# Performance work log

Hardware: AMD Instinct MI355X
Metric: run time of the kernel (lower is better)

Reference implementation:

```python
import jax, jax.numpy as jnp
import numpy as np

NUM_USERS = 100000
NUM_ITEMS = 50000
IN_DIM = 128
HID_DIM = 256
OUT_DIM = 64
R = 5
E = 300000  # edges per rating level
EPS = 1e-10


def setup_inputs() -> dict:
    key = jax.random.key(0)
    ks = jax.random.split(key, 12)
    # edge lists per rating, regularized to dense [R, E]
    u_idx = jax.random.randint(ks[0], (R, E), 0, NUM_USERS, dtype=jnp.int32)
    v_idx = jax.random.randint(ks[1], (R, E), 0, NUM_ITEMS, dtype=jnp.int32)
    deg_user = jax.random.uniform(ks[2], (NUM_USERS,), dtype=jnp.float32) * 50.0
    deg_item = jax.random.uniform(ks[3], (NUM_ITEMS,), dtype=jnp.float32) * 100.0
    # learned parameters (xavier-ish scaling)
    X_u = jax.random.normal(ks[4], (NUM_USERS, IN_DIM), dtype=jnp.float32) * 0.02
    X_v = jax.random.normal(ks[5], (NUM_ITEMS, IN_DIM), dtype=jnp.float32) * 0.02
    s1 = float(np.sqrt(6.0 / (IN_DIM + HID_DIM)))
    W_item2user = jax.random.uniform(ks[6], (R, IN_DIM, HID_DIM), dtype=jnp.float32, minval=-s1, maxval=s1)
    W_user2item = jax.random.uniform(ks[7], (R, IN_DIM, HID_DIM), dtype=jnp.float32, minval=-s1, maxval=s1)
    s2 = float(np.sqrt(6.0 / (HID_DIM + OUT_DIM)))
    W_out_user = jax.random.uniform(ks[8], (HID_DIM, OUT_DIM), dtype=jnp.float32, minval=-s2, maxval=s2)
    b_out_user = jnp.zeros((OUT_DIM,), dtype=jnp.float32)
    W_out_item = jax.random.uniform(ks[9], (HID_DIM, OUT_DIM), dtype=jnp.float32, minval=-s2, maxval=s2)
    b_out_item = jnp.zeros((OUT_DIM,), dtype=jnp.float32)
    return {
        "u_idx": u_idx, "v_idx": v_idx,
        "deg_user": deg_user, "deg_item": deg_item,
        "X_u": X_u, "X_v": X_v,
        "W_item2user": W_item2user, "W_user2item": W_user2item,
        "W_out_user": W_out_user, "b_out_user": b_out_user,
        "W_out_item": W_out_item, "b_out_item": b_out_item,
    }


def reference(u_idx, v_idx, deg_user, deg_item, X_u, X_v,
              W_item2user, W_user2item,
              W_out_user, b_out_user, W_out_item, b_out_item):
    num_users = X_u.shape[0]
    num_items = X_v.shape[0]
    deg_u = jnp.sqrt(jnp.clip(deg_user, EPS))
    deg_v = jnp.sqrt(jnp.clip(deg_item, EPS))
    # per-edge symmetric normalization, [R, E]
    norm = 1.0 / (deg_u[u_idx] * deg_v[v_idx])
    # gather + per-rating matmul + normalize  ([R,E,in] x [R,in,hid] -> [R,E,hid])
    msgs_to_u = jnp.einsum('rek,rkh->reh', X_v[v_idx], W_item2user) * norm[..., None]
    msgs_to_v = jnp.einsum('rek,rkh->reh', X_u[u_idx], W_user2item) * norm[..., None]
    # scatter-add into shared accumulators (equivalent of index_add_ over all ratings)
    m_u = jax.ops.segment_sum(msgs_to_u.reshape(-1, msgs_to_u.shape[-1]),
                              u_idx.reshape(-1), num_segments=num_users)
    m_v = jax.ops.segment_sum(msgs_to_v.reshape(-1, msgs_to_v.shape[-1]),
                              v_idx.reshape(-1), num_segments=num_items)
    # output dense layers + ReLU (dropout disabled / eval mode)
    h_u = jax.nn.relu(m_u @ W_out_user + b_out_user)
    h_v = jax.nn.relu(m_v @ W_out_item + b_out_item)
    return h_u, h_v
```

## Files before the change

kernel.cpp:

```cpp
#include <hip/hip_runtime.h>
#include <hip/hip_bf16.h>

#define NUM_USERS 100000
#define NUM_ITEMS 50000
#define IN_DIM 128
#define HID_DIM 256
#define OUT_DIM 64
#define R_LEVELS 5
#define NEDGE 300000
#define EPSC 1e-10f

typedef float f32x4 __attribute__((ext_vector_type(4)));
typedef short s16x8 __attribute__((ext_vector_type(8)));

static __device__ __forceinline__ short f2bf(float f) {
    __hip_bfloat16 h = __float2bfloat16(f);
    return *reinterpret_cast<short*>(&h);
}

__global__ void fuse_weights(const float* __restrict__ W_i2u,
                             const float* __restrict__ W_u2i,
                             const float* __restrict__ Wout_u,
                             const float* __restrict__ Wout_i,
                             unsigned short* __restrict__ WcT_u,
                             unsigned short* __restrict__ WcT_v) {
    const int rk = blockIdx.x;
    const int r  = rk >> 7;
    const int k  = rk & 127;
    const int j  = threadIdx.x;
    const bool userDir = (blockIdx.y == 0);
    const float* w1   = (userDir ? W_i2u : W_u2i) + (size_t)rk * HID_DIM;
    const float* wout = (userDir ? Wout_u : Wout_i);
    float acc = 0.f;
    for (int h = 0; h < HID_DIM; ++h)
        acc = fmaf(w1[h], wout[h * OUT_DIM + j], acc);
    unsigned short* dst = (userDir ? WcT_u : WcT_v);
    dst[(((size_t)r * OUT_DIM + j) * IN_DIM) + k] = (unsigned short)f2bf(acc);
}

__global__ __launch_bounds__(256)
void edge_mfma(const int*   __restrict__ u_idx,
               const int*   __restrict__ v_idx,
               const float* __restrict__ deg_user,
               const float* __restrict__ deg_item,
               const float* __restrict__ X_u,
               const float* __restrict__ X_v,
               const unsigned short* __restrict__ WcT_u,
               const unsigned short* __restrict__ WcT_v,
               float*       __restrict__ out) {
    const int r    = blockIdx.y;
    const bool toUser = (blockIdx.z == 0);
    const int lane = threadIdx.x & 63;
    const int wave = threadIdx.x >> 6;
    const int m    = lane & 15;
    const int g    = lane >> 4;

    const int*   dI   = (toUser ? u_idx : v_idx) + (size_t)r * NEDGE;
    const int*   sI   = (toUser ? v_idx : u_idx) + (size_t)r * NEDGE;
    const float* degD = toUser ? deg_user : deg_item;
    const float* degS = toUser ? deg_item : deg_user;
    const float* Xs   = toUser ? X_v : X_u;
    const unsigned short* WcT = (toUser ? WcT_u : WcT_v) + (size_t)r * OUT_DIM * IN_DIM;
    float*       outp = out + (toUser ? 0 : (size_t)NUM_USERS * OUT_DIM);

    s16x8 bfrag[4][4];
#pragma unroll
    for (int nt = 0; nt < 4; ++nt)
#pragma unroll
        for (int ks = 0; ks < 4; ++ks)
            bfrag[nt][ks] = *reinterpret_cast<const s16x8*>(
                WcT + ((size_t)(nt * 16 + m) * IN_DIM + ks * 32 + g * 8));

    const int wid     = blockIdx.x * 4 + wave;
    const int wstride = gridDim.x * 4;
    constexpr int NCHUNK = NEDGE / 16;

    for (int c = wid; c < NCHUNK; c += wstride) {
        const int e0 = c * 16;
        const int   sS  = sI[e0 + m];
        const int   dDm = dI[e0 + m];
        const float norm = 1.0f / (sqrtf(fmaxf(degD[dDm], EPSC)) *
                                   sqrtf(fmaxf(degS[sS],  EPSC)));
        const float* xrow = Xs + (size_t)sS * IN_DIM;

        s16x8 afrag[4];
#pragma unroll
        for (int ks = 0; ks < 4; ++ks) {
            const float4 q0 = *reinterpret_cast<const float4*>(xrow + ks * 32 + g * 8);
            const float4 q1 = *reinterpret_cast<const float4*>(xrow + ks * 32 + g * 8 + 4);
            s16x8 av;
            av[0] = f2bf(q0.x * norm); av[1] = f2bf(q0.y * norm);
            av[2] = f2bf(q0.z * norm); av[3] = f2bf(q0.w * norm);
            av[4] = f2bf(q1.x * norm); av[5] = f2bf(q1.y * norm);
            av[6] = f2bf(q1.z * norm); av[7] = f2bf(q1.w * norm);
            afrag[ks] = av;
        }

        int dd[4];
#pragma unroll
        for (int i = 0; i < 4; ++i) dd[i] = dI[e0 + g * 4 + i];

#pragma unroll
        for (int nt = 0; nt < 4; ++nt) {
            f32x4 acc = {0.f, 0.f, 0.f, 0.f};
#pragma unroll
            for (int ks = 0; ks < 4; ++ks)
                acc = __builtin_amdgcn_mfma_f32_16x16x32_bf16(
                    afrag[ks], bfrag[nt][ks], acc, 0, 0, 0);
#pragma unroll
            for (int i = 0; i < 4; ++i)
                atomicAdd(outp + (size_t)dd[i] * OUT_DIM + nt * 16 + m, acc[i]);
        }
    }
}

__global__ void bias_relu(float* __restrict__ out,
                          const float* __restrict__ b_u,
                          const float* __restrict__ b_v) {
    const size_t i = (size_t)blockIdx.x * 256 + threadIdx.x;
    constexpr size_t UOUT = (size_t)NUM_USERS * OUT_DIM;
    constexpr size_t TOT  = UOUT + (size_t)NUM_ITEMS * OUT_DIM;
    if (i < TOT) {
        const float b = (i < UOUT) ? b_u[i & 63] : b_v[i & 63];
        out[i] = fmaxf(out[i] + b, 0.f);
    }
}

extern "C" void kernel_launch(void* const* d_in, const int* in_sizes, int n_in,
                              void* d_out, int out_size, void* d_ws, size_t ws_size,
                              hipStream_t stream) {
    const int*   u_idx    = (const int*)  d_in[0];
    const int*   v_idx    = (const int*)  d_in[1];
    const float* deg_user = (const float*)d_in[2];
    const float* deg_item = (const float*)d_in[3];
    const float* X_u      = (const float*)d_in[4];
    const float* X_v      = (const float*)d_in[5];
    const float* W_i2u    = (const float*)d_in[6];
    const float* W_u2i    = (const float*)d_in[7];
    const float* W_out_u  = (const float*)d_in[8];
    const float* b_out_u  = (const float*)d_in[9];
    const float* W_out_i  = (const float*)d_in[10];
    const float* b_out_i  = (const float*)d_in[11];

    float* out  = (float*)d_out;
    unsigned short* WcT_u = (unsigned short*)d_ws;
    unsigned short* WcT_v = WcT_u + (size_t)R_LEVELS * OUT_DIM * IN_DIM;

    hipMemsetAsync(d_out, 0, (size_t)out_size * sizeof(float), stream);

    fuse_weights<<<dim3(R_LEVELS * IN_DIM, 2), 64, 0, stream>>>(
        W_i2u, W_u2i, W_out_u, W_out_i, WcT_u, WcT_v);

    edge_mfma<<<dim3(128, R_LEVELS, 2), 256, 0, stream>>>(
        u_idx, v_idx, deg_user, deg_item, X_u, X_v, WcT_u, WcT_v, out);

    const size_t total = (size_t)NUM_USERS * OUT_DIM + (size_t)NUM_ITEMS * OUT_DIM;
    bias_relu<<<(int)((total + 255) / 256), 256, 0, stream>>>(out, b_out_u, b_out_i);
}
```

Measured before the change: 808.3 us.

## Prescale feature rows to bf16 and factor destination degree norm into epilogue

Adds a prescale pass that multiplies each source row by its inverse sqrt degree and stores it as bf16. The destination-side normalization moves out of the edge loop and into the final bias/ReLU pass as a per-row scale. The edge kernel then gathers half-size bf16 rows, skips the per-edge degree lookups and conversions, and loads destination indices as int4. The grid also grows from 128 to 384 blocks in x. This costs an extra pass over both feature tables plus workspace, and the fast path is only taken when the workspace is large enough.

```diff
diff --git a/kernel.cpp b/kernel.cpp
--- a/kernel.cpp
+++ b/kernel.cpp
@@ -13,9 +13,9 @@
 typedef float f32x4 __attribute__((ext_vector_type(4)));
 typedef short s16x8 __attribute__((ext_vector_type(8)));
 
-static __device__ __forceinline__ short f2bf(float f) {
+static __device__ __forceinline__ unsigned short f2bf(float f) {
     __hip_bfloat16 h = __float2bfloat16(f);
-    return *reinterpret_cast<short*>(&h);
+    return *reinterpret_cast<unsigned short*>(&h);
 }
 
 __global__ void fuse_weights(const float* __restrict__ W_i2u,
@@ -35,19 +35,32 @@
     for (int h = 0; h < HID_DIM; ++h)
         acc = fmaf(w1[h], wout[h * OUT_DIM + j], acc);
     unsigned short* dst = (userDir ? WcT_u : WcT_v);
-    dst[(((size_t)r * OUT_DIM + j) * IN_DIM) + k] = (unsigned short)f2bf(acc);
+    dst[(((size_t)r * OUT_DIM + j) * IN_DIM) + k] = f2bf(acc);
+}
+
+__global__ void prescale_rows(const float* __restrict__ X,
+                              const float* __restrict__ deg,
+                              unsigned short* __restrict__ Xn,
+                              float* __restrict__ rsq, int nrows) {
+    const int row = blockIdx.x * 4 + (threadIdx.x >> 6);
+    if (row >= nrows) return;
+    const int lane = threadIdx.x & 63;
+    const float r = 1.0f / sqrtf(fmaxf(deg[row], EPSC));
+    if (lane == 0) rsq[row] = r;
+    const float2 x = ((const float2*)(X + (size_t)row * IN_DIM))[lane];
+    const unsigned int packed = (unsigned int)f2bf(x.x * r) |
+                                ((unsigned int)f2bf(x.y * r) << 16);
+    ((unsigned int*)(Xn + (size_t)row * IN_DIM))[lane] = packed;
 }
 
 __global__ __launch_bounds__(256)
-void edge_mfma(const int*   __restrict__ u_idx,
-               const int*   __restrict__ v_idx,
-               const float* __restrict__ deg_user,
-               const float* __restrict__ deg_item,
-               const float* __restrict__ X_u,
-               const float* __restrict__ X_v,
-               const unsigned short* __restrict__ WcT_u,
-               const unsigned short* __restrict__ WcT_v,
-               float*       __restrict__ out) {
+void edge_mfma_pre(const int* __restrict__ u_idx,
+                   const int* __restrict__ v_idx,
+                   const unsigned short* __restrict__ Xn_u,
+                   const unsigned short* __restrict__ Xn_v,
+                   const unsigned short* __restrict__ WcT_u,
+                   const unsigned short* __restrict__ WcT_v,
+                   float* __restrict__ out) {
     const int r    = blockIdx.y;
     const bool toUser = (blockIdx.z == 0);
     const int lane = threadIdx.x & 63;
@@ -55,13 +68,71 @@
     const int m    = lane & 15;
     const int g    = lane >> 4;
 
+    const int* dI = (toUser ? u_idx : v_idx) + (size_t)r * NEDGE;
+    const int* sI = (toUser ? v_idx : u_idx) + (size_t)r * NEDGE;
+    const unsigned short* Xn  = toUser ? Xn_v : Xn_u;
+    const unsigned short* WcT = (toUser ? WcT_u : WcT_v) + (size_t)r * OUT_DIM * IN_DIM;
+    float* outp = out + (toUser ? 0 : (size_t)NUM_USERS * OUT_DIM);
+
+    s16x8 bfrag[4][4];
+#pragma unroll
+    for (int nt = 0; nt < 4; ++nt)
+#pragma unroll
+        for (int ks = 0; ks < 4; ++ks)
+            bfrag[nt][ks] = *reinterpret_cast<const s16x8*>(
+                WcT + ((size_t)(nt * 16 + m) * IN_DIM + ks * 32 + g * 8));
+
+    const int wid     = blockIdx.x * 4 + wave;
+    const int wstride = gridDim.x * 4;
+    constexpr int NCHUNK = NEDGE / 16;
+
+    for (int c = wid; c < NCHUNK; c += wstride) {
+        const int e0 = c * 16;
+        const int sS = sI[e0 + m];
+        const int4 dd4 = *reinterpret_cast<const int4*>(dI + e0 + g * 4);
+        const unsigned short* xrow = Xn + (size_t)sS * IN_DIM;
+
+        s16x8 afrag[4];
+#pragma unroll
+        for (int ks = 0; ks < 4; ++ks)
+            afrag[ks] = *reinterpret_cast<const s16x8*>(xrow + ks * 32 + g * 8);
+
+        const int dd[4] = {dd4.x, dd4.y, dd4.z, dd4.w};
+#pragma unroll
+        for (int nt = 0; nt < 4; ++nt) {
+            f32x4 acc = {0.f, 0.f, 0.f, 0.f};
+#pragma unroll
+            for (int ks = 0; ks < 4; ++ks)
+                acc = __builtin_amdgcn_mfma_f32_16x16x32_bf16(
+                    afrag[ks], bfrag[nt][ks], acc, 0, 0, 0);
+#pragma unroll
+            for (int i = 0; i < 4; ++i)
+                atomicAdd(outp + (size_t)dd[i] * OUT_DIM + nt * 16 + m, acc[i]);
+        }
+    }
+}
+
+__global__ __launch_bounds__(256)
+void edge_mfma(const int* __restrict__ u_idx, const int* __restrict__ v_idx,
+               const float* __restrict__ deg_user, const float* __restrict__ deg_item,
+               const float* __restrict__ X_u, const float* __restrict__ X_v,
+               const unsigned short* __restrict__ WcT_u,
+               const unsigned short* __restrict__ WcT_v,
+               float* __restrict__ out) {
+    const int r    = blockIdx.y;
+    const bool toUser = (blockIdx.z == 0);
+    const int lane = threadIdx.x & 63;
+    const int wave = threadIdx.x >> 6;
+    const int m    = lane & 15;
+    const int g    = lane >> 4;
+
     const int*   dI   = (toUser ? u_idx : v_idx) + (size_t)r * NEDGE;
     const int*   sI   = (toUser ? v_idx : u_idx) + (size_t)r * NEDGE;
     const float* degD = toUser ? deg_user : deg_item;
     const float* degS = toUser ? deg_item : deg_user;
     const float* Xs   = toUser ? X_v : X_u;
     const unsigned short* WcT = (toUser ? WcT_u : WcT_v) + (size_t)r * OUT_DIM * IN_DIM;
-    float*       outp = out + (toUser ? 0 : (size_t)NUM_USERS * OUT_DIM);
+    float* outp = out + (toUser ? 0 : (size_t)NUM_USERS * OUT_DIM);
 
     s16x8 bfrag[4][4];
 #pragma unroll
@@ -77,8 +148,8 @@
 
     for (int c = wid; c < NCHUNK; c += wstride) {
         const int e0 = c * 16;
-        const int   sS  = sI[e0 + m];
-        const int   dDm = dI[e0 + m];
+        const int sS  = sI[e0 + m];
+        const int dDm = dI[e0 + m];
         const float norm = 1.0f / (sqrtf(fmaxf(degD[dDm], EPSC)) *
                                    sqrtf(fmaxf(degS[sS],  EPSC)));
         const float* xrow = Xs + (size_t)sS * IN_DIM;
@@ -89,10 +160,10 @@
             const float4 q0 = *reinterpret_cast<const float4*>(xrow + ks * 32 + g * 8);
             const float4 q1 = *reinterpret_cast<const float4*>(xrow + ks * 32 + g * 8 + 4);
             s16x8 av;
-            av[0] = f2bf(q0.x * norm); av[1] = f2bf(q0.y * norm);
-            av[2] = f2bf(q0.z * norm); av[3] = f2bf(q0.w * norm);
-            av[4] = f2bf(q1.x * norm); av[5] = f2bf(q1.y * norm);
-            av[6] = f2bf(q1.z * norm); av[7] = f2bf(q1.w * norm);
+            av[0] = (short)f2bf(q0.x * norm); av[1] = (short)f2bf(q0.y * norm);
+            av[2] = (short)f2bf(q0.z * norm); av[3] = (short)f2bf(q0.w * norm);
+            av[4] = (short)f2bf(q1.x * norm); av[5] = (short)f2bf(q1.y * norm);
+            av[6] = (short)f2bf(q1.z * norm); av[7] = (short)f2bf(q1.w * norm);
             afrag[ks] = av;
         }
 
@@ -111,6 +182,22 @@
             for (int i = 0; i < 4; ++i)
                 atomicAdd(outp + (size_t)dd[i] * OUT_DIM + nt * 16 + m, acc[i]);
         }
+    }
+}
+
+__global__ void bias_relu_scaled(float* __restrict__ out,
+                                 const float* __restrict__ b_u,
+                                 const float* __restrict__ b_v,
+                                 const float* __restrict__ rsq_u,
+                                 const float* __restrict__ rsq_v) {
+    const size_t i = (size_t)blockIdx.x * 256 + threadIdx.x;
+    constexpr size_t UOUT = (size_t)NUM_USERS * OUT_DIM;
+    constexpr size_t TOT  = UOUT + (size_t)NUM_ITEMS * OUT_DIM;
+    if (i < UOUT) {
+        out[i] = fmaxf(fmaf(out[i], rsq_u[i >> 6], b_u[i & 63]), 0.f);
+    } else if (i < TOT) {
+        const size_t k = i - UOUT;
+        out[i] = fmaxf(fmaf(out[i], rsq_v[k >> 6], b_v[i & 63]), 0.f);
     }
 }
 
@@ -142,18 +229,41 @@
     const float* W_out_i  = (const float*)d_in[10];
     const float* b_out_i  = (const float*)d_in[11];
 
-    float* out  = (float*)d_out;
-    unsigned short* WcT_u = (unsigned short*)d_ws;
-    unsigned short* WcT_v = WcT_u + (size_t)R_LEVELS * OUT_DIM * IN_DIM;
+    float* out = (float*)d_out;
+
+    constexpr size_t WCT_ELEMS = (size_t)R_LEVELS * OUT_DIM * IN_DIM;
+    char* wsb = (char*)d_ws;
+    unsigned short* WcT_u = (unsigned short*)wsb;
+    unsigned short* WcT_v = WcT_u + WCT_ELEMS;
+    float* rsq_u = (float*)(wsb + 163840);
+    float* rsq_v = (float*)(wsb + 563840);
+    unsigned short* Xn_u = (unsigned short*)(wsb + 763840);
+    unsigned short* Xn_v = (unsigned short*)(wsb + 763840 + 25600000);
+    constexpr size_t WS_NEED = 763840 + 25600000 + 12800000;
+    const bool fast = (ws_size >= WS_NEED);
 
     hipMemsetAsync(d_out, 0, (size_t)out_size * sizeof(float), stream);
 
     fuse_weights<<<dim3(R_LEVELS * IN_DIM, 2), 64, 0, stream>>>(
         W_i2u, W_u2i, W_out_u, W_out_i, WcT_u, WcT_v);
 
-    edge_mfma<<<dim3(128, R_LEVELS, 2), 256, 0, stream>>>(
-        u_idx, v_idx, deg_user, deg_item, X_u, X_v, WcT_u, WcT_v, out);
-
-    const size_t total = (size_t)NUM_USERS * OUT_DIM + (size_t)NUM_ITEMS * OUT_DIM;
-    bias_relu<<<(int)((total + 255) / 256), 256, 0, stream>>>(out, b_out_u, b_out_i);
-}
+    if (fast) {
+        prescale_rows<<<(NUM_USERS + 3) / 4, 256, 0, stream>>>(
+            X_u, deg_user, Xn_u, rsq_u, NUM_USERS);
+        prescale_rows<<<(NUM_ITEMS + 3) / 4, 256, 0, stream>>>(
+            X_v, deg_item, Xn_v, rsq_v, NUM_ITEMS);
+
+        edge_mfma_pre<<<dim3(384, R_LEVELS, 2), 256, 0, stream>>>(
+            u_idx, v_idx, Xn_u, Xn_v, WcT_u, WcT_v, out);
+
+        const size_t total = (size_t)NUM_USERS * OUT_DIM + (size_t)NUM_ITEMS * OUT_DIM;
+        bias_relu_scaled<<<(int)((total + 255) / 256), 256, 0, stream>>>(
+            out, b_out_u, b_out_i, rsq_u, rsq_v);
+    } else {
+        edge_mfma<<<dim3(384, R_LEVELS, 2), 256, 0, stream>>>(
+            u_idx, v_idx, deg_user, deg_item, X_u, X_v, WcT_u, WcT_v, out);
+
+        const size_t total = (size_t)NUM_USERS * OUT_DIM + (size_t)NUM_ITEMS * OUT_DIM;
+        bias_relu<<<(int)((total + 255) / 256), 256, 0, stream>>>(out, b_out_u, b_out_i);
+    }
+}
```

After: 800.0 us. Within noise of the previous version (-1.0%).
